# Performance work log

Measured on AMD Instinct MI355X. Metric: run time of the kernel, lower is better.

Reference implementation:

```python
import jax, jax.numpy as jnp
import numpy as np

K = 32  # top-k along the feature dim


def setup_inputs() -> dict:
    key = jax.random.key(0)
    B, S, D = 8, 4096, 1024
    x = jax.random.normal(key, (B, S, D), dtype=jnp.float32)
    return {
        "x": x,
        "log_alpha": jnp.zeros((), dtype=jnp.float32),
        "log_sigma": jnp.zeros((), dtype=jnp.float32),
        "ema_mean": jnp.zeros((D,), dtype=jnp.float32),
        "ema_sq": jnp.ones((D,), dtype=jnp.float32),
    }


def reference(x, log_alpha, log_sigma, ema_mean, ema_sq):
    # base = exact (erf) GELU, matching torch.nn.GELU default
    base = jax.nn.gelu(x, approximate=False)
    # per-channel z-score using EMA stats
    ema_var = jnp.clip(ema_sq - ema_mean ** 2, 1e-6, None)
    z_abs = jnp.abs(x - ema_mean) * jax.lax.rsqrt(ema_var)  # [B,S,D]
    # surprise = mean of top-K |z| along feature dim
    top_vals, _ = jax.lax.top_k(z_abs, K)                    # [B,S,K]
    surp = jnp.mean(top_vals, axis=-1, keepdims=True)        # [B,S,1]
    gate = 1.0 + jnp.exp(log_alpha) * jnp.tanh(jnp.exp(log_sigma) * surp)
    return base * gate
```

## Files before the change

kernel.cpp:

```cpp
#include <hip/hip_runtime.h>
#include <math.h>

#define D 1024
#define TOPK 32
#define VPT 16
#define WPB 4
#define BITER 7

typedef float vfloat4 __attribute__((ext_vector_type(4)));

__device__ __forceinline__ float fast_gelu(float x) {
  const float x2 = x * x;
  const float p = __builtin_fmaf(0.044715f, x2, 1.0f);
  const float a = -1.5957691216f * x * p;
  const float e = __expf(a);
  const float r = __builtin_amdgcn_rcpf(1.0f + e);
  return x * r;
}

__device__ __forceinline__ float fast_tanh_pos(float y) {
  const float e = __expf(-2.0f * y);
  return (1.0f - e) * __builtin_amdgcn_rcpf(1.0f + e);
}

#define DPP_ADD_F32(v, ctrl)                                                   \
  v += __int_as_float(                                                         \
      __builtin_amdgcn_update_dpp(0, __float_as_int(v), ctrl, 0xf, 0xf, true))

__device__ __forceinline__ float waveSumDpp(float v) {
  DPP_ADD_F32(v, 0x111);
  DPP_ADD_F32(v, 0x112);
  DPP_ADD_F32(v, 0x114);
  DPP_ADD_F32(v, 0x118);
  DPP_ADD_F32(v, 0x142);
  DPP_ADD_F32(v, 0x143);
  return __int_as_float(__builtin_amdgcn_readlane(__float_as_int(v), 63));
}

__global__ __launch_bounds__(256) void prep_stats(const float* __restrict__ ema_mean,
                                                  const float* __restrict__ ema_sq,
                                                  const float* __restrict__ p_la,
                                                  const float* __restrict__ p_ls,
                                                  float* __restrict__ ws) {
  int i = blockIdx.x * 256 + threadIdx.x;
  if (i < D) {
    float m = ema_mean[i];
    float v = ema_sq[i] - m * m;
    ws[i] = rsqrtf(fmaxf(v, 1e-6f));
  }
  if (i == 0) {
    ws[D] = expf(p_la[0]);
    ws[D + 1] = expf(p_ls[0]);
  }
}

__global__ __launch_bounds__(256, 4) void gelu_gate(const float* __restrict__ x,
                                                    const float* __restrict__ ema_mean,
                                                    const float* __restrict__ ws,
                                                    float* __restrict__ out,
                                                    int n_rows) {
  const int wave = threadIdx.x >> 6;
  const int lane = threadIdx.x & 63;
  const int row = blockIdx.x * WPB + wave;
  if (row >= n_rows) return;
  const float* __restrict__ xr = x + (size_t)row * D;

  float4 a[4], mm[4], ss[4];
#pragma unroll
  for (int j = 0; j < 4; ++j)
    a[j] = *reinterpret_cast<const float4*>(xr + j * 256 + lane * 4);
#pragma unroll
  for (int j = 0; j < 4; ++j) {
    mm[j] = *reinterpret_cast<const float4*>(ema_mean + j * 256 + lane * 4);
    ss[j] = *reinterpret_cast<const float4*>(ws + j * 256 + lane * 4);
  }
  const float alpha = ws[D];
  const float sigma = ws[D + 1];

  float za[VPT];
#pragma unroll
  for (int j = 0; j < 4; ++j) {
    za[4 * j + 0] = fabsf(a[j].x - mm[j].x) * ss[j].x;
    za[4 * j + 1] = fabsf(a[j].y - mm[j].y) * ss[j].y;
    za[4 * j + 2] = fabsf(a[j].z - mm[j].z) * ss[j].z;
    za[4 * j + 3] = fabsf(a[j].w - mm[j].w) * ss[j].w;
  }

  float lo = 0.0f, hi = 16.0f;
#pragma unroll
  for (int it = 0; it < BITER; ++it) {
    const float mid = 0.5f * (lo + hi);
    int c = 0;
#pragma unroll
    for (int i = 0; i < VPT; ++i)
      c += (int)__popcll(__ballot(za[i] >= mid));
    const bool g = (c >= TOPK);
    lo = g ? mid : lo;
    hi = g ? hi : mid;
  }
  const float t = lo;

  float s = 0.0f;
#pragma unroll
  for (int i = 0; i < VPT; ++i) s += fmaxf(za[i] - t, 0.0f);
  s = waveSumDpp(s);
  const float surp = (s + (float)TOPK * t) * (1.0f / (float)TOPK);
  const float gate = 1.0f + alpha * fast_tanh_pos(sigma * surp);

  float* __restrict__ orow = out + (size_t)row * D;
#pragma unroll
  for (int j = 0; j < 4; ++j) {
    vfloat4 o;
    o.x = fast_gelu(a[j].x) * gate;
    o.y = fast_gelu(a[j].y) * gate;
    o.z = fast_gelu(a[j].z) * gate;
    o.w = fast_gelu(a[j].w) * gate;
    __builtin_nontemporal_store(o, reinterpret_cast<vfloat4*>(orow + j * 256 + lane * 4));
  }
}

extern "C" void kernel_launch(void* const* d_in, const int* in_sizes, int n_in,
                              void* d_out, int out_size, void* d_ws, size_t ws_size,
                              hipStream_t stream) {
  const float* x    = (const float*)d_in[0];
  const float* la   = (const float*)d_in[1];
  const float* ls   = (const float*)d_in[2];
  const float* mean = (const float*)d_in[3];
  const float* sq   = (const float*)d_in[4];
  float* out = (float*)d_out;
  float* ws = (float*)d_ws;

  const int n = in_sizes[0];
  const int n_rows = n / D;

  prep_stats<<<(D + 255) / 256, 256, 0, stream>>>(mean, sq, la, ls, ws);

  const int grid = (n_rows + WPB - 1) / WPB;
  gelu_gate<<<grid, WPB * 64, 0, stream>>>(x, mean, ws, out, n_rows);
}
```

Measured before the change: 234.3 us.

## Use persistent waves with double-buffered row prefetch in gelu_gate

Launches a fixed grid of 1024 blocks, where each wave processes a contiguous chunk of rows instead of exactly one row. Each row's loads are prefetched into alternating register buffers, so the next row's global load overlaps the current row's top-k threshold search and GELU computation. The per-channel mean and scale loads are amortized across all rows a wave handles. The cost is higher register pressure from the two buffers, which may reduce occupancy, and fewer waves in flight to hide memory latency.

```diff
diff --git a/kernel.cpp b/kernel.cpp
--- a/kernel.cpp
+++ b/kernel.cpp
@@ -5,6 +5,7 @@
 #define TOPK 32
 #define VPT 16
 #define WPB 4
+#define NBLK 1024
 #define BITER 7
 
 typedef float vfloat4 __attribute__((ext_vector_type(4)));
@@ -61,61 +62,84 @@
                                                     int n_rows) {
   const int wave = threadIdx.x >> 6;
   const int lane = threadIdx.x & 63;
-  const int row = blockIdx.x * WPB + wave;
-  if (row >= n_rows) return;
-  const float* __restrict__ xr = x + (size_t)row * D;
+  const int col = lane * 4;
+  const int gw = blockIdx.x * WPB + wave;
+  const int nw = NBLK * WPB;
+  const int rpw = (n_rows + nw - 1) / nw;
+  int r0 = gw * rpw;
+  if (r0 >= n_rows) return;
+  const int r_end = min(r0 + rpw, n_rows);
 
-  float4 a[4], mm[4], ss[4];
-#pragma unroll
-  for (int j = 0; j < 4; ++j)
-    a[j] = *reinterpret_cast<const float4*>(xr + j * 256 + lane * 4);
+  float4 mm[4], ss[4];
 #pragma unroll
   for (int j = 0; j < 4; ++j) {
-    mm[j] = *reinterpret_cast<const float4*>(ema_mean + j * 256 + lane * 4);
-    ss[j] = *reinterpret_cast<const float4*>(ws + j * 256 + lane * 4);
+    mm[j] = *reinterpret_cast<const float4*>(ema_mean + j * 256 + col);
+    ss[j] = *reinterpret_cast<const float4*>(ws + j * 256 + col);
   }
   const float alpha = ws[D];
   const float sigma = ws[D + 1];
 
-  float za[VPT];
+  float4 A[4], B[4];
+
+  auto prefetch = [&](float4(&buf)[4], int row) {
+    if (row < r_end) {
+      const float* __restrict__ xr = x + (size_t)row * D;
 #pragma unroll
-  for (int j = 0; j < 4; ++j) {
-    za[4 * j + 0] = fabsf(a[j].x - mm[j].x) * ss[j].x;
-    za[4 * j + 1] = fabsf(a[j].y - mm[j].y) * ss[j].y;
-    za[4 * j + 2] = fabsf(a[j].z - mm[j].z) * ss[j].z;
-    za[4 * j + 3] = fabsf(a[j].w - mm[j].w) * ss[j].w;
-  }
+      for (int j = 0; j < 4; ++j)
+        buf[j] = *reinterpret_cast<const float4*>(xr + j * 256 + col);
+    }
+  };
 
-  float lo = 0.0f, hi = 16.0f;
+  auto process = [&](const float4(&a)[4], int row) {
+    if (row >= r_end) return;
+    float za[VPT];
 #pragma unroll
-  for (int it = 0; it < BITER; ++it) {
-    const float mid = 0.5f * (lo + hi);
-    int c = 0;
+    for (int j = 0; j < 4; ++j) {
+      za[4 * j + 0] = fabsf(a[j].x - mm[j].x) * ss[j].x;
+      za[4 * j + 1] = fabsf(a[j].y - mm[j].y) * ss[j].y;
+      za[4 * j + 2] = fabsf(a[j].z - mm[j].z) * ss[j].z;
+      za[4 * j + 3] = fabsf(a[j].w - mm[j].w) * ss[j].w;
+    }
+
+    float lo = 0.0f, hi = 16.0f;
 #pragma unroll
-    for (int i = 0; i < VPT; ++i)
-      c += (int)__popcll(__ballot(za[i] >= mid));
-    const bool g = (c >= TOPK);
-    lo = g ? mid : lo;
-    hi = g ? hi : mid;
-  }
-  const float t = lo;
+    for (int it = 0; it < BITER; ++it) {
+      const float mid = 0.5f * (lo + hi);
+      int c = 0;
+#pragma unroll
+      for (int i = 0; i < VPT; ++i)
+        c += (int)__popcll(__ballot(za[i] >= mid));
+      const bool g = (c >= TOPK);
+      lo = g ? mid : lo;
+      hi = g ? hi : mid;
+    }
+    const float t = lo;
 
-  float s = 0.0f;
+    float s = 0.0f;
 #pragma unroll
-  for (int i = 0; i < VPT; ++i) s += fmaxf(za[i] - t, 0.0f);
-  s = waveSumDpp(s);
-  const float surp = (s + (float)TOPK * t) * (1.0f / (float)TOPK);
-  const float gate = 1.0f + alpha * fast_tanh_pos(sigma * surp);
+    for (int i = 0; i < VPT; ++i) s += fmaxf(za[i] - t, 0.0f);
+    s = waveSumDpp(s);
+    const float surp = (s + (float)TOPK * t) * (1.0f / (float)TOPK);
+    const float gate = 1.0f + alpha * fast_tanh_pos(sigma * surp);
 
-  float* __restrict__ orow = out + (size_t)row * D;
+    float* __restrict__ orow = out + (size_t)row * D;
 #pragma unroll
-  for (int j = 0; j < 4; ++j) {
-    vfloat4 o;
-    o.x = fast_gelu(a[j].x) * gate;
-    o.y = fast_gelu(a[j].y) * gate;
-    o.z = fast_gelu(a[j].z) * gate;
-    o.w = fast_gelu(a[j].w) * gate;
-    __builtin_nontemporal_store(o, reinterpret_cast<vfloat4*>(orow + j * 256 + lane * 4));
+    for (int j = 0; j < 4; ++j) {
+      vfloat4 o;
+      o.x = fast_gelu(a[j].x) * gate;
+      o.y = fast_gelu(a[j].y) * gate;
+      o.z = fast_gelu(a[j].z) * gate;
+      o.w = fast_gelu(a[j].w) * gate;
+      __builtin_nontemporal_store(o, reinterpret_cast<vfloat4*>(orow + j * 256 + col));
+    }
+  };
+
+  prefetch(A, r0);
+  for (int r = r0; r < r_end; r += 2) {
+    prefetch(B, r + 1);
+    process(A, r);
+    prefetch(A, r + 2);
+    process(B, r + 1);
   }
 }
 
@@ -135,6 +159,5 @@
 
   prep_stats<<<(D + 255) / 256, 256, 0, stream>>>(mean, sq, la, ls, ws);
 
-  const int grid = (n_rows + WPB - 1) / WPB;
-  gelu_gate<<<grid, WPB * 64, 0, stream>>>(x, mean, ws, out, n_rows);
+  gelu_gate<<<NBLK, WPB * 64, 0, stream>>>(x, mean, ws, out, n_rows);
 }
```

New measurement: 247.8 us. 5.8% more time.
